# Kernel optimization log

Measured on AMD Instinct MI355X. Metric: run time of the kernel, lower is better.

Reference implementation:

```python
import jax, jax.numpy as jnp
import numpy as np

R, CH, N, E, C, OUT, ED = 2, 2, 20000, 100000, 256, 256, 16


def setup_inputs() -> dict:
    key = jax.random.key(0)
    ks = jax.random.split(key, 11)
    inv = 1.0 / np.sqrt(C)
    return {
        "x": jax.random.normal(ks[0], (R * CH * N, C), jnp.float32),
        "edge_attr": jax.random.normal(ks[1], (E, ED), jnp.float32),
        "edge_weight": jax.random.uniform(ks[2], (R, CH, E, 1), jnp.float32),
        "lin_W": jax.random.normal(ks[3], (C, C), jnp.float32) * inv,
        "lin_b": jax.random.normal(ks[4], (C,), jnp.float32) * inv,
        "linl_W": jax.random.normal(ks[5], (C, OUT), jnp.float32) * inv,
        "linl_b": jax.random.normal(ks[6], (OUT,), jnp.float32) * inv,
        "linr_W": jax.random.normal(ks[7], (C, OUT), jnp.float32) * inv,
        "bond_W": jax.random.normal(ks[8], (ED, C), jnp.float32) / np.sqrt(ED),
        "bond_b": jax.random.normal(ks[9], (C,), jnp.float32) / np.sqrt(ED),
        "edge_index": jax.random.randint(ks[10], (2, E), 0, N, jnp.int64),
    }


def reference(x, edge_attr, edge_weight, lin_W, lin_b, linl_W, linl_b, linr_W,
              bond_W, bond_b, edge_index):
    # bond encoder: (E, ED) -> (E, C), broadcasts as (1, 1, E, C)
    edge_emb = edge_attr @ bond_W + bond_b
    x_l = x @ lin_W + lin_b                      # (R*CH*N, C)
    ux = x_l.reshape(R, CH, N, C)
    src = edge_index[0]
    dst = edge_index[1]
    # gather + add + GELU (exact/erf, matching torch F.gelu) + weight
    msg = jax.nn.gelu(ux[:, :, src, :] + edge_emb, approximate=False) * edge_weight  # (R,CH,E,C)
    # scatter_mean over edge targets
    sums = jnp.zeros((R, CH, N, C), x.dtype).at[:, :, dst, :].add(msg)
    cnt = jnp.zeros((N,), x.dtype).at[dst].add(1.0)
    out = sums / jnp.maximum(cnt, 1.0)[None, None, :, None]
    out = out.reshape(-1, C)                     # (R*CH*N, C)
    return out @ linl_W + linl_b + x @ linr_W
```

## Files before the change

### kernel.cpp

```cpp
#include <hip/hip_runtime.h>
#include <math.h>

#define NN 20000
#define EE 100000
#define CC 256
#define EDM 16
#define RC 4
#define MTOT (RC * NN)
#define PREPB ((EE + 255) / 256)
#define CONVB 10000

typedef __attribute__((ext_vector_type(8))) short short8;
typedef __attribute__((ext_vector_type(4))) float floatx4;

__device__ __forceinline__ unsigned short f2bf(float f) {
    union { float f; unsigned u; } v; v.f = f;
    unsigned r = v.u + 0x7FFF + ((v.u >> 16) & 1);
    return (unsigned short)(r >> 16);
}
__device__ __forceinline__ float uif(unsigned u) {
    union { unsigned u; float f; } v; v.u = u;
    return v.f;
}

__device__ __forceinline__ float gelu27(float v) {
    const float z  = fabsf(v) * 0.70710678118654752f;
    const float P  = fmaf(z, fmaf(z, fmaf(z, fmaf(z, 0.078108f, 0.000972f),
                           0.230389f), 0.278393f), 1.0f);
    const float r  = __builtin_amdgcn_rcpf(P);
    const float r2 = r * r;
    const float r4 = r2 * r2;
    const float h  = 0.5f * fabsf(v);
    return fmaf(0.5f, v, fmaf(-h, r4, h));
}

#define GLDS16(gp, lp)                                                        \
    __builtin_amdgcn_global_load_lds(                                         \
        (const __attribute__((address_space(1))) unsigned int*)(gp),          \
        (__attribute__((address_space(3))) unsigned int*)(lp), 16, 0, 0)

__global__ void k_prep(const float* __restrict__ lin_W,
                       const float* __restrict__ linl_W,
                       const float* __restrict__ linr_W,
                       unsigned short* __restrict__ linWT,
                       unsigned short* __restrict__ WbT,
                       const int* __restrict__ eidx,
                       int* __restrict__ cnt,
                       const float* __restrict__ x,
                       unsigned short* __restrict__ xb) {
    const int b = blockIdx.x;
    const int t = threadIdx.x;
    if (b < CC) {
        linWT[b * CC + t]      = f2bf(lin_W[t * CC + b]);
        WbT[b * 512 + t]       = f2bf(linl_W[t * CC + b]);
        WbT[b * 512 + 256 + t] = f2bf(linr_W[t * CC + b]);
    } else if (b < CC + PREPB) {
        int e = (b - CC) * 256 + t;
        if (e < EE) atomicAdd(cnt + eidx[EE + e], 1);
    } else {
        const size_t i8 = (size_t)(b - CC - PREPB) * 2048 + t * 8;
        const float4 v0 = *(const float4*)(x + i8);
        const float4 v1 = *(const float4*)(x + i8 + 4);
        uint4 p;
        p.x = (unsigned)f2bf(v0.x) | ((unsigned)f2bf(v0.y) << 16);
        p.y = (unsigned)f2bf(v0.z) | ((unsigned)f2bf(v0.w) << 16);
        p.z = (unsigned)f2bf(v1.x) | ((unsigned)f2bf(v1.y) << 16);
        p.w = (unsigned)f2bf(v1.z) | ((unsigned)f2bf(v1.w) << 16);
        *(uint4*)(xb + i8) = p;
    }
}

template <int XB>
__global__ __launch_bounds__(512, 4) void k_mm1(const float* __restrict__ xf,
                                                const unsigned short* __restrict__ xb,
                                                const unsigned short* __restrict__ linWT,
                                                const float* __restrict__ lin_b,
                                                unsigned short* __restrict__ xlb4) {
    __shared__ __attribute__((aligned(16))) char SH[33280];
    unsigned short* As = (unsigned short*)SH;
    unsigned short* Bs = As + 128 * 64;
    const int tid  = threadIdx.x;
    const int lane = tid & 63;
    const int wave = tid >> 6;
    const int wr   = wave >> 2;
    const int wc   = wave & 3;
    const int l15  = lane & 15;
    const int q4   = lane >> 4;
    const int lr8  = lane >> 3;
    const int lc8  = lane & 7;
    const int sc8  = (lc8 ^ lr8) * 8;
    const int nn0  = blockIdx.x * 32;
    const int n0   = blockIdx.y * 128;

    floatx4 acc[4][2];
#pragma unroll
    for (int mt = 0; mt < 4; mt++)
#pragma unroll
        for (int nt = 0; nt < 2; nt++) acc[mt][nt] = (floatx4)0.0f;

    for (int kc = 0; kc < 256; kc += 64) {
        __syncthreads();
#pragma unroll
        for (int it = 0; it < 2; it++) {
            const int op = wave * 2 + it;
            GLDS16(linWT + (size_t)(n0 + op * 8 + lr8) * CC + kc + sc8,
                   Bs + op * 512);
        }
        if (XB) {
#pragma unroll
            for (int it = 0; it < 2; it++) {
                const int op = wave * 2 + it;
                const int r  = op * 8 + lr8;
                const int grow = (r >> 5) * NN + nn0 + (r & 31);
                GLDS16(xb + (size_t)grow * CC + kc + sc8, As + op * 512);
            }
        } else {
#pragma unroll
            for (int w = 0; w < 2; w++) {
                const int q  = w * 512 + tid;
                const int r  = q >> 3;
                const int c8 = q & 7;
                const int grow = (r >> 5) * NN + nn0 + (r & 31);
                const float* s = xf + (size_t)grow * CC + kc + c8 * 8;
                float4 v0 = *(const float4*)(s);
                float4 v1 = *(const float4*)(s + 4);
                uint4 p;
                p.x = (unsigned)f2bf(v0.x) | ((unsigned)f2bf(v0.y) << 16);
                p.y = (unsigned)f2bf(v0.z) | ((unsigned)f2bf(v0.w) << 16);
                p.z = (unsigned)f2bf(v1.x) | ((unsigned)f2bf(v1.y) << 16);
                p.w = (unsigned)f2bf(v1.z) | ((unsigned)f2bf(v1.w) << 16);
                *(uint4*)(As + r * 64 + ((c8 ^ (r & 7)) * 8)) = p;
            }
        }
        __syncthreads();
#pragma unroll
        for (int kk = 0; kk < 64; kk += 32) {
            short8 a[4], b[2];
#pragma unroll
            for (int mt = 0; mt < 4; mt++) {
                const int row = wr * 64 + mt * 16 + l15;
                a[mt] = *(const short8*)(As + row * 64 +
                                         ((kk + q4 * 8) ^ ((row & 7) * 8)));
            }
#pragma unroll
            for (int nt = 0; nt < 2; nt++) {
                const int row = wc * 32 + nt * 16 + l15;
                b[nt] = *(const short8*)(Bs + row * 64 +
                                         ((kk + q4 * 8) ^ ((row & 7) * 8)));
            }
#pragma unroll
            for (int mt = 0; mt < 4; mt++)
#pragma unroll
                for (int nt = 0; nt < 2; nt++)
                    acc[mt][nt] = __builtin_amdgcn_mfma_f32_16x16x32_bf16(
                        a[mt], b[nt], acc[mt][nt], 0, 0, 0);
        }
    }
    __syncthreads();
    char* E = SH;
#pragma unroll
    for (int nt = 0; nt < 2; nt++) {
        const int cl = wc * 32 + nt * 16 + l15;
        const float bz = lin_b[n0 + cl];
#pragma unroll
        for (int m0 = 0; m0 < 2; m0++) {
#pragma unroll
            for (int rr = 0; rr < 4; rr++) {
                const int i = m0 * 16 + q4 * 4 + rr;
                const unsigned lo = f2bf(acc[m0][nt][rr] + bz);
                const unsigned hi = f2bf(acc[m0 + 2][nt][rr] + bz);
                *(unsigned*)(E + i * 1040 + cl * 8 + wr * 4) = lo | (hi << 16);
            }
        }
    }
    __syncthreads();
    char* gb = (char*)xlb4 + (size_t)nn0 * 2048 + (size_t)n0 * 8;
#pragma unroll
    for (int p = 0; p < 4; p++) {
        const int idx = p * 512 + tid;
        const int i   = idx >> 6;
        const int w   = (idx & 63) * 16;
        uint4 v = *(const uint4*)(E + i * 1040 + w);
        *(uint4*)(gb + (size_t)i * 2048 + w) = v;
    }
}

template <int XB>
__global__ __launch_bounds__(512, 4) void k_mm2(const unsigned short* __restrict__ mean_b,
                                                const unsigned short* __restrict__ xb,
                                                const float* __restrict__ xf,
                                                const unsigned short* __restrict__ WbT,
                                                const float* __restrict__ bias,
                                                float* __restrict__ out) {
    __shared__ unsigned short As[128 * 64];
    __shared__ unsigned short Bs[128 * 64];
    const int tid  = threadIdx.x;
    const int lane = tid & 63;
    const int wave = tid >> 6;
    const int wr   = wave >> 2;
    const int wc   = wave & 3;
    const int l15  = lane & 15;
    const int q4   = lane >> 4;
    const int lr8  = lane >> 3;
    const int lc8  = lane & 7;
    const int sc8  = (lc8 ^ lr8) * 8;
    const int i0   = blockIdx.x * 128;
    const int n0   = blockIdx.y * 128;

    floatx4 acc[4][2];
#pragma unroll
    for (int mt = 0; mt < 4; mt++)
#pragma unroll
        for (int nt = 0; nt < 2; nt++) acc[mt][nt] = (floatx4)0.0f;

    for (int kc = 0; kc < 512; kc += 64) {
        __syncthreads();
        const int first = (kc < 256);
        const int kco   = first ? kc : kc - 256;
#pragma unroll
        for (int it = 0; it < 2; it++) {
            const int op = wave * 2 + it;
            GLDS16(WbT + (size_t)(n0 + op * 8 + lr8) * 512 + kc + sc8,
                   Bs + op * 512);
        }
        if (first || XB) {
            const unsigned short* ab = first ? mean_b : xb;
#pragma unroll
            for (int it = 0; it < 2; it++) {
                const int op = wave * 2 + it;
                GLDS16(ab + (size_t)(i0 + op * 8 + lr8) * CC + kco + sc8,
                       As + op * 512);
            }
        } else {
#pragma unroll
            for (int w = 0; w < 2; w++) {
                const int q  = w * 512 + tid;
                const int r  = q >> 3;
                const int c8 = q & 7;
                const float* s = xf + (size_t)(i0 + r) * CC + kco + c8 * 8;
                float4 v0 = *(const float4*)(s);
                float4 v1 = *(const float4*)(s + 4);
                uint4 p;
                p.x = (unsigned)f2bf(v0.x) | ((unsigned)f2bf(v0.y) << 16);
                p.y = (unsigned)f2bf(v0.z) | ((unsigned)f2bf(v0.w) << 16);
                p.z = (unsigned)f2bf(v1.x) | ((unsigned)f2bf(v1.y) << 16);
                p.w = (unsigned)f2bf(v1.z) | ((unsigned)f2bf(v1.w) << 16);
                *(uint4*)(As + r * 64 + ((c8 ^ (r & 7)) * 8)) = p;
            }
        }
        __syncthreads();
#pragma unroll
        for (int kk = 0; kk < 64; kk += 32) {
            short8 a[4], b[2];
#pragma unroll
            for (int mt = 0; mt < 4; mt++) {
                const int row = wr * 64 + mt * 16 + l15;
                a[mt] = *(const short8*)(As + row * 64 +
                                         ((kk + q4 * 8) ^ ((row & 7) * 8)));
            }
#pragma unroll
            for (int nt = 0; nt < 2; nt++) {
                const int row = wc * 32 + nt * 16 + l15;
                b[nt] = *(const short8*)(Bs + row * 64 +
                                         ((kk + q4 * 8) ^ ((row & 7) * 8)));
            }
#pragma unroll
            for (int mt = 0; mt < 4; mt++)
#pragma unroll
                for (int nt = 0; nt < 2; nt++)
                    acc[mt][nt] = __builtin_amdgcn_mfma_f32_16x16x32_bf16(
                        a[mt], b[nt], acc[mt][nt], 0, 0, 0);
        }
    }
#pragma unroll
    for (int nt = 0; nt < 2; nt++) {
        const int col = n0 + wc * 32 + nt * 16 + l15;
        const float bz = bias[col];
#pragma unroll
        for (int mt = 0; mt < 4; mt++) {
#pragma unroll
            for (int rr = 0; rr < 4; rr++) {
                const int row = i0 + wr * 64 + mt * 16 + q4 * 4 + rr;
                out[(size_t)row * CC + col] = acc[mt][nt][rr] + bz;
            }
        }
    }
}

#define SCAN_T 1024
#define SCHUNK 20
__global__ __launch_bounds__(1024) void k_scan(const int* __restrict__ cnt,
                                               int* __restrict__ offs,
                                               int* __restrict__ cursor) {
    __shared__ int ps[SCAN_T];
    const int t = threadIdx.x;
    const int base = t * SCHUNK;
    int s = 0;
#pragma unroll
    for (int i = 0; i < SCHUNK; i++) {
        int idx = base + i;
        if (idx < NN) s += cnt[idx];
    }
    ps[t] = s;
    __syncthreads();
    for (int off = 1; off < SCAN_T; off <<= 1) {
        int v = (t >= off) ? ps[t - off] : 0;
        __syncthreads();
        ps[t] += v;
        __syncthreads();
    }
    int excl = (t == 0) ? 0 : ps[t - 1];
#pragma unroll
    for (int i = 0; i < SCHUNK; i++) {
        int idx = base + i;
        if (idx < NN) {
            offs[idx]   = excl;
            cursor[idx] = excl;
            excl += cnt[idx];
        }
    }
    if (t == SCAN_T - 1) offs[NN] = ps[SCAN_T - 1];
}

__global__ void k_scatter(const int* __restrict__ eidx,
                          const float* __restrict__ ew,
                          int* __restrict__ cursor,
                          int* __restrict__ bucket,
                          int* __restrict__ srcb,
                          float4* __restrict__ ewb) {
    int e = blockIdx.x * 256 + threadIdx.x;
    if (e < EE) {
        int d = eidx[EE + e];
        int p = atomicAdd(cursor + d, 1);
        bucket[p] = e;
        srcb[p]   = eidx[e];
        ewb[p]    = make_float4(ew[e], ew[EE + e], ew[2 * EE + e], ew[3 * EE + e]);
    }
}

__global__ __launch_bounds__(256) void k_agg(const unsigned short* __restrict__ xlb4,
                                             const float* __restrict__ edge_attr,
                                             const float4* __restrict__ ewb,
                                             const float* __restrict__ bond_W,
                                             const float* __restrict__ bond_b,
                                             const int* __restrict__ srcb,
                                             const int* __restrict__ offs,
                                             const int* __restrict__ bucket,
                                             unsigned short* __restrict__ mean_b) {
    const int n = blockIdx.x;
    const int c = threadIdx.x;
    const int beg = offs[n], end = offs[n + 1];
    const float bb = bond_b[c];
    float bw[EDM];
#pragma unroll
    for (int k = 0; k < EDM; k++) bw[k] = bond_W[k * CC + c];

    float a0 = 0.f, a1 = 0.f, a2 = 0.f, a3 = 0.f;

#pragma unroll 2
    for (int j = beg; j < end; j++) {
        const int e     = bucket[j];
        const int src   = srcb[j];
        const float4 w  = ewb[j];
        const float4* ea4 = (const float4*)(edge_attr + (size_t)e * EDM);
        const float4 q0 = ea4[0], q1 = ea4[1], q2 = ea4[2], q3 = ea4[3];
        float emb = bb;
        emb = fmaf(q0.x, bw[0],  emb); emb = fmaf(q0.y, bw[1],  emb);
        emb = fmaf(q0.z, bw[2],  emb); emb = fmaf(q0.w, bw[3],  emb);
        emb = fmaf(q1.x, bw[4],  emb); emb = fmaf(q1.y, bw[5],  emb);
        emb = fmaf(q1.z, bw[6],  emb); emb = fmaf(q1.w, bw[7],  emb);
        emb = fmaf(q2.x, bw[8],  emb); emb = fmaf(q2.y, bw[9],  emb);
        emb = fmaf(q2.z, bw[10], emb); emb = fmaf(q2.w, bw[11], emb);
        emb = fmaf(q3.x, bw[12], emb); emb = fmaf(q3.y, bw[13], emb);
        emb = fmaf(q3.z, bw[14], emb); emb = fmaf(q3.w, bw[15], emb);
        const uint2 u = *(const uint2*)(xlb4 + ((size_t)src * CC + c) * 4);
        const float v0 = uif(u.x << 16)          + emb;
        const float v1 = uif(u.x & 0xffff0000u)  + emb;
        const float v2 = uif(u.y << 16)          + emb;
        const float v3 = uif(u.y & 0xffff0000u)  + emb;
        a0 = fmaf(gelu27(v0), w.x, a0);
        a1 = fmaf(gelu27(v1), w.y, a1);
        a2 = fmaf(gelu27(v2), w.z, a2);
        a3 = fmaf(gelu27(v3), w.w, a3);
    }
    const float inv = 1.0f / fmaxf((float)(end - beg), 1.0f);
    const size_t ob = (size_t)n * CC + c;
    mean_b[ob]                       = f2bf(a0 * inv);
    mean_b[ob + (size_t)NN * CC]     = f2bf(a1 * inv);
    mean_b[ob + (size_t)2 * NN * CC] = f2bf(a2 * inv);
    mean_b[ob + (size_t)3 * NN * CC] = f2bf(a3 * inv);
}

extern "C" void kernel_launch(void* const* d_in, const int* in_sizes, int n_in,
                              void* d_out, int out_size, void* d_ws, size_t ws_size,
                              hipStream_t stream) {
    (void)in_sizes; (void)n_in; (void)out_size;
    const float* x           = (const float*)d_in[0];
    const float* edge_attr   = (const float*)d_in[1];
    const float* edge_weight = (const float*)d_in[2];
    const float* lin_W       = (const float*)d_in[3];
    const float* lin_b       = (const float*)d_in[4];
    const float* linl_W      = (const float*)d_in[5];
    const float* linl_b      = (const float*)d_in[6];
    const float* linr_W      = (const float*)d_in[7];
    const float* bond_W      = (const float*)d_in[8];
    const float* bond_b      = (const float*)d_in[9];
    const int*   edge_index  = (const int*)d_in[10];

    unsigned short* xlb4  = (unsigned short*)d_ws;
    unsigned short* linWT = xlb4 + (size_t)MTOT * CC;
    unsigned short* WbT   = linWT + CC * CC;
    int* cnt    = (int*)(WbT + CC * 512);
    int* offs   = cnt + NN;
    int* cursor = offs + NN + 1;
    int* bucket = cursor + NN;
    uintptr_t mb_addr = (((uintptr_t)(bucket + EE)) + 255) & ~(uintptr_t)255;
    unsigned short* mean_b = (unsigned short*)mb_addr;
    unsigned short* xb     = mean_b + (size_t)MTOT * CC;
    const size_t need_xb = ((uintptr_t)(xb + (size_t)MTOT * CC)) - (uintptr_t)d_ws;
    const int use_xb = (ws_size >= need_xb);

    float4* ewb  = (float4*)d_out;
    int*    srcb = (int*)(ewb + EE);

    hipMemsetAsync(cnt, 0, NN * sizeof(int), stream);

    k_prep<<<CC + PREPB + (use_xb ? CONVB : 0), 256, 0, stream>>>(
        lin_W, linl_W, linr_W, linWT, WbT, edge_index, cnt, x,
        use_xb ? xb : nullptr);
    if (use_xb)
        k_mm1<1><<<dim3(NN / 32, 2), 512, 0, stream>>>(nullptr, xb, linWT, lin_b, xlb4);
    else
        k_mm1<0><<<dim3(NN / 32, 2), 512, 0, stream>>>(x, nullptr, linWT, lin_b, xlb4);
    k_scan<<<1, SCAN_T, 0, stream>>>(cnt, offs, cursor);
    k_scatter<<<PREPB, 256, 0, stream>>>(edge_index, edge_weight,
                                         cursor, bucket, srcb, ewb);
    k_agg<<<NN, 256, 0, stream>>>(xlb4, edge_attr, ewb, bond_W, bond_b,
                                  srcb, offs, bucket, mean_b);
    if (use_xb)
        k_mm2<1><<<dim3(MTOT / 128, 2), 512, 0, stream>>>(
            mean_b, xb, nullptr, WbT, linl_b, (float*)d_out);
    else
        k_mm2<0><<<dim3(MTOT / 128, 2), 512, 0, stream>>>(
            mean_b, nullptr, x, WbT, linl_b, (float*)d_out);
}
```

Before: 345.0 us.

## Precompute bond edge embeddings in separate kernel stored as fp16 in bucket order

Moves the per-edge bond-encoder matvec out of the aggregation loop into a new kernel that writes an fp16 embedding per edge in destination-sorted bucket order, staged in the output buffer. The aggregation kernel then streams a contiguous fp16 value per channel instead of gathering edge_attr and redoing 16 FMAs per edge. It also uses pointer-increment and shift-based addressing for the gathers. The cost is an extra 51 MB write plus read and one more launch, fp16 rounding of the embedding, and reliance on d_out being large enough for scratch space before k_mm2 overwrites it.

```diff
diff --git a/kernel.cpp b/kernel.cpp
--- a/kernel.cpp
+++ b/kernel.cpp
@@ -9,6 +9,7 @@
 #define MTOT (RC * NN)
 #define PREPB ((EE + 255) / 256)
 #define CONVB 10000
+#define JB 64
 
 typedef __attribute__((ext_vector_type(8))) short short8;
 typedef __attribute__((ext_vector_type(4))) float floatx4;
@@ -21,6 +22,14 @@
 __device__ __forceinline__ float uif(unsigned u) {
     union { unsigned u; float f; } v; v.u = u;
     return v.f;
+}
+__device__ __forceinline__ unsigned short f2h(float f) {
+    union { _Float16 h; unsigned short u; } v; v.h = (_Float16)f;
+    return v.u;
+}
+__device__ __forceinline__ float h2f(unsigned short u) {
+    union { unsigned short u; _Float16 h; } v; v.u = u;
+    return (float)v.h;
 }
 
 __device__ __forceinline__ float gelu27(float v) {
@@ -338,46 +347,60 @@
     }
 }
 
-__global__ __launch_bounds__(256) void k_agg(const unsigned short* __restrict__ xlb4,
+__global__ __launch_bounds__(256) void k_emb(const int* __restrict__ bucket,
                                              const float* __restrict__ edge_attr,
-                                             const float4* __restrict__ ewb,
                                              const float* __restrict__ bond_W,
                                              const float* __restrict__ bond_b,
+                                             unsigned short* __restrict__ embb) {
+    const int c = threadIdx.x;
+    float bw[EDM];
+#pragma unroll
+    for (int k = 0; k < EDM; k++) bw[k] = bond_W[k * CC + c];
+    const float bb = bond_b[c];
+    const int j0   = blockIdx.x * JB;
+    const int jend = (j0 + JB < EE) ? (j0 + JB) : EE;
+#pragma unroll 2
+    for (int j = j0; j < jend; j++) {
+        const int e = bucket[j];
+        const float4* ea4 = (const float4*)(edge_attr + (size_t)e * EDM);
+        const float4 q0 = ea4[0], q1 = ea4[1], q2 = ea4[2], q3 = ea4[3];
+        float s0 = fmaf(q0.x, bw[0],  fmaf(q0.y, bw[1],  fmaf(q0.z, bw[2],  q0.w * bw[3])));
+        float s1 = fmaf(q1.x, bw[4],  fmaf(q1.y, bw[5],  fmaf(q1.z, bw[6],  q1.w * bw[7])));
+        float s2 = fmaf(q2.x, bw[8],  fmaf(q2.y, bw[9],  fmaf(q2.z, bw[10], q2.w * bw[11])));
+        float s3 = fmaf(q3.x, bw[12], fmaf(q3.y, bw[13], fmaf(q3.z, bw[14], q3.w * bw[15])));
+        embb[(size_t)j * CC + c] = f2h(bb + ((s0 + s1) + (s2 + s3)));
+    }
+}
+
+__global__ __launch_bounds__(256) void k_agg(const unsigned short* __restrict__ xlb4,
+                                             const unsigned short* __restrict__ embb,
+                                             const float4* __restrict__ ewb,
                                              const int* __restrict__ srcb,
                                              const int* __restrict__ offs,
-                                             const int* __restrict__ bucket,
                                              unsigned short* __restrict__ mean_b) {
     const int n = blockIdx.x;
     const int c = threadIdx.x;
     const int beg = offs[n], end = offs[n + 1];
-    const float bb = bond_b[c];
-    float bw[EDM];
-#pragma unroll
-    for (int k = 0; k < EDM; k++) bw[k] = bond_W[k * CC + c];
+    const char* xl = (const char*)xlb4;
+    const unsigned cw = (unsigned)c << 3;
+
+    const int*            sp = srcb + beg;
+    const float4*         wp = ewb + beg;
+    const unsigned short* ep = embb + (size_t)beg * CC + c;
 
     float a0 = 0.f, a1 = 0.f, a2 = 0.f, a3 = 0.f;
 
 #pragma unroll 2
     for (int j = beg; j < end; j++) {
-        const int e     = bucket[j];
-        const int src   = srcb[j];
-        const float4 w  = ewb[j];
-        const float4* ea4 = (const float4*)(edge_attr + (size_t)e * EDM);
-        const float4 q0 = ea4[0], q1 = ea4[1], q2 = ea4[2], q3 = ea4[3];
-        float emb = bb;
-        emb = fmaf(q0.x, bw[0],  emb); emb = fmaf(q0.y, bw[1],  emb);
-        emb = fmaf(q0.z, bw[2],  emb); emb = fmaf(q0.w, bw[3],  emb);
-        emb = fmaf(q1.x, bw[4],  emb); emb = fmaf(q1.y, bw[5],  emb);
-        emb = fmaf(q1.z, bw[6],  emb); emb = fmaf(q1.w, bw[7],  emb);
-        emb = fmaf(q2.x, bw[8],  emb); emb = fmaf(q2.y, bw[9],  emb);
-        emb = fmaf(q2.z, bw[10], emb); emb = fmaf(q2.w, bw[11], emb);
-        emb = fmaf(q3.x, bw[12], emb); emb = fmaf(q3.y, bw[13], emb);
-        emb = fmaf(q3.z, bw[14], emb); emb = fmaf(q3.w, bw[15], emb);
-        const uint2 u = *(const uint2*)(xlb4 + ((size_t)src * CC + c) * 4);
-        const float v0 = uif(u.x << 16)          + emb;
-        const float v1 = uif(u.x & 0xffff0000u)  + emb;
-        const float v2 = uif(u.y << 16)          + emb;
-        const float v3 = uif(u.y & 0xffff0000u)  + emb;
+        const int src      = *sp++;
+        const float4 w     = *wp++;
+        const float emf    = h2f(*ep);
+        ep += CC;
+        const uint2 u = *(const uint2*)(xl + (((unsigned)src << 11) + cw));
+        const float v0 = uif(u.x << 16)          + emf;
+        const float v1 = uif(u.x & 0xffff0000u)  + emf;
+        const float v2 = uif(u.y << 16)          + emf;
+        const float v3 = uif(u.y & 0xffff0000u)  + emf;
         a0 = fmaf(gelu27(v0), w.x, a0);
         a1 = fmaf(gelu27(v1), w.y, a1);
         a2 = fmaf(gelu27(v2), w.z, a2);
@@ -422,6 +445,7 @@
 
     float4* ewb  = (float4*)d_out;
     int*    srcb = (int*)(ewb + EE);
+    unsigned short* embb = (unsigned short*)((char*)d_out + 2000128);
 
     hipMemsetAsync(cnt, 0, NN * sizeof(int), stream);
 
@@ -435,8 +459,9 @@
     k_scan<<<1, SCAN_T, 0, stream>>>(cnt, offs, cursor);
     k_scatter<<<PREPB, 256, 0, stream>>>(edge_index, edge_weight,
                                          cursor, bucket, srcb, ewb);
-    k_agg<<<NN, 256, 0, stream>>>(xlb4, edge_attr, ewb, bond_W, bond_b,
-                                  srcb, offs, bucket, mean_b);
+    k_emb<<<(EE + JB - 1) / JB, 256, 0, stream>>>(bucket, edge_attr, bond_W,
+                                                  bond_b, embb);
+    k_agg<<<NN, 256, 0, stream>>>(xlb4, embb, ewb, srcb, offs, mean_b);
     if (use_xb)
         k_mm2<1><<<dim3(MTOT / 128, 2), 512, 0, stream>>>(
             mean_b, xb, nullptr, WbT, linl_b, (float*)d_out);
```

Measured after the change: 353.2 us. 2.4% more time.
